# Kernel tuning notes

Hardware: AMD Instinct MI355X
Metric: run time of the kernel (lower is better)

Reference implementation:

```python
import jax, jax.numpy as jnp
import numpy as np
import math

def setup_inputs() -> dict:
    key = jax.random.key(0)
    qkv = jax.random.normal(key, (64, 192, 2048), dtype=jnp.float32)
    return {"qkv": qkv}

def reference(qkv):
    # qkv: [N, 3C, T]
    ch = qkv.shape[1] // 3
    q, k, v = jnp.split(qkv, 3, axis=1)  # each [N, C, T]
    scale = 1.0 / math.sqrt(math.sqrt(ch))
    # scores: [N, T, S]
    weight = jnp.einsum('bct,bcs->bts', q * scale, k * scale)
    weight = jax.nn.softmax(weight.astype(jnp.float32), axis=-1).astype(qkv.dtype)
    return jnp.einsum('bts,bcs->bct', weight, v)  # [N, C, T]
```

## Files before the change

### kernel.cpp

```cpp
#include <hip/hip_runtime.h>
#include <hip/hip_bf16.h>

typedef __attribute__((ext_vector_type(16))) float    f32x16;
typedef __attribute__((ext_vector_type(8)))  short    s16x8;
typedef __attribute__((ext_vector_type(2)))  unsigned u32x2;

#define NB    64
#define CH    64
#define TS    2048
#define QBLK  256
#define KVB   64
#define NKV   (TS / KVB)
#define KT_OFF  (16u * 1024 * 1024)
#define V_OFF   (32u * 1024 * 1024)
#define BSTRIDE (TS * CH * 2)
#define QSCALE  0.18033688011112042f

__device__ __forceinline__ unsigned f2bf(float f) {
    unsigned u = __float_as_uint(f);
    return (u + 0x7fffu + ((u >> 16) & 1u)) >> 16;
}
__device__ __forceinline__ unsigned cvtpk(float lo, float hi) {
    unsigned r;
    asm("v_cvt_pk_bf16_f32 %0, %1, %2" : "=v"(r) : "v"(lo), "v"(hi));
    return r;
}
__device__ __forceinline__ u32x2 plswap(unsigned x, unsigned y) {
#if __has_builtin(__builtin_amdgcn_permlane32_swap)
    return __builtin_amdgcn_permlane32_swap(x, y, false, false);
#else
    asm("v_permlane32_swap_b32 %0, %1" : "+v"(x), "+v"(y));
    u32x2 r; r.x = x; r.y = y; return r;
#endif
}
__device__ __forceinline__ float crosshalf_sum(float x) {
    const u32x2 r = plswap(__float_as_uint(x), __float_as_uint(x));
    return __uint_as_float(r.x) + __uint_as_float(r.y);
}
__device__ __forceinline__ void gload16(const void* g, void* l) {
    __builtin_amdgcn_global_load_lds(
        (const __attribute__((address_space(1))) void*)g,
        (__attribute__((address_space(3))) void*)l, 16, 0, 0);
}

__global__ __launch_bounds__(256)
void prep_all(const float* __restrict__ qkv, char* __restrict__ ws)
{
    __shared__ float tile[64][65];
    const int bid = (int)blockIdx.x;
    if (bid < NB * 32) {
        const int b  = bid >> 5;
        const int tt = bid & 31;
        const float* src = qkv + ((size_t)b * 192 + 64) * TS + tt * 64;

        const int c  = threadIdx.x >> 2;
        const int tq = (threadIdx.x & 3) * 16;
        const float4* s4 = (const float4*)(src + (size_t)c * TS + tq);
        #pragma unroll
        for (int j = 0; j < 4; ++j) {
            const float4 f = s4[j];
            tile[c][tq + 4*j + 0] = f.x;
            tile[c][tq + 4*j + 1] = f.y;
            tile[c][tq + 4*j + 2] = f.z;
            tile[c][tq + 4*j + 3] = f.w;
        }
        __syncthreads();

        const int t  = threadIdx.x >> 2;
        const int cq = (threadIdx.x & 3) * 16;
        unsigned pk[8];
        #pragma unroll
        for (int j = 0; j < 8; ++j) {
            const float f0 = tile[cq + 2*j][t];
            const float f1 = tile[cq + 2*j + 1][t];
            pk[j] = f2bf(f0) | (f2bf(f1) << 16);
        }
        char* dst = ws + KT_OFF +
                    (size_t)b * BSTRIDE + ((size_t)tt * 64 + t) * 128 + cq * 2;
        ((uint4*)dst)[0] = make_uint4(pk[0], pk[1], pk[2], pk[3]);
        ((uint4*)dst)[1] = make_uint4(pk[4], pk[5], pk[6], pk[7]);
    } else {
        const size_t e   = ((size_t)(bid - NB * 32) * 256 + threadIdx.x) * 16;
        const int b      = (int)(e >> 17);
        const size_t rem = e & 131071;
        const float4* src = (const float4*)(qkv + (size_t)b * 393216 + 262144 + rem);
        unsigned pk[8];
        #pragma unroll
        for (int j = 0; j < 4; ++j) {
            const float4 f = src[j];
            pk[2*j]     = f2bf(f.x) | (f2bf(f.y) << 16);
            pk[2*j + 1] = f2bf(f.z) | (f2bf(f.w) << 16);
        }
        char* dst = ws + V_OFF + e * 2;
        ((uint4*)dst)[0] = make_uint4(pk[0], pk[1], pk[2], pk[3]);
        ((uint4*)dst)[1] = make_uint4(pk[4], pk[5], pk[6], pk[7]);
    }
}

template<bool DIRA>
__device__ __forceinline__ void attn_main(
    const float* __restrict__ qsrcB, const char* __restrict__ ktb,
    const char* __restrict__ vtb, float* __restrict__ ob,
    char* k_sm0, char* k_sm1, char* v_sm0, char* v_sm1,
    int t0, int lane, int wv, int tid)
{
    const int col = lane & 31;
    const int hi  = lane >> 5;

    const int rowb = tid >> 3;
    const unsigned offX = (unsigned)(((tid & 7) ^ (rowb & 7)) << 4);
    const char* ksrc = ktb + rowb * 128  + offX;
    const char* vsrc = vtb + rowb * 4096 + offX;
    char* kd0 = k_sm0 + tid * 16;
    char* vd0 = v_sm0 + tid * 16;
    char* kd1 = k_sm1 + tid * 16;
    char* vd1 = v_sm1 + tid * 16;

    gload16(ksrc, kd0);
    gload16(vsrc, vd0);

    s16x8 qfrag[4];
    {
        const int t = t0 + wv * 32 + col;
        const float* qs = qsrcB + t;
        #pragma unroll
        for (int ks = 0; ks < 4; ++ks) {
            union { unsigned u[4]; s16x8 v; } qq;
            #pragma unroll
            for (int m = 0; m < 4; ++m) {
                const int c = ks * 16 + hi * 8 + 2 * m;
                const float a = qs[(size_t)c * TS]       * QSCALE;
                const float b = qs[(size_t)(c + 1) * TS] * QSCALE;
                qq.u[m] = cvtpk(a, b);
            }
            qfrag[ks] = qq.v;
        }
    }

    f32x16 zf;
    f32x16 oacc0, oacc1;
    #pragma unroll
    for (int i = 0; i < 16; ++i) { zf[i] = 0.f; oacc0[i] = 0.f; oacc1[i] = 0.f; }
    float l_run = 0.f;

    __syncthreads();

    int cur = 0;
    for (int kt = 0; kt < NKV; ++kt) {
        if (kt + 1 < NKV) {
            gload16(ksrc + (size_t)(kt + 1) * 8192, cur ? kd0 : kd1);
            gload16(vsrc + (size_t)(kt + 1) * 128,  cur ? vd0 : vd1);
        }
        const char* kb = cur ? k_sm1 : k_sm0;
        const char* vb = cur ? v_sm1 : v_sm0;

        f32x16 sa0, sa1;
        __builtin_amdgcn_s_setprio(1);
        #pragma unroll
        for (int ks = 0; ks < 4; ++ks) {
            const int sw = 32 * ks + 16 * hi;
            const s16x8 kf0 = *(const s16x8*)(kb + col * 128        + (sw ^ ((col & 7) << 4)));
            const s16x8 kf1 = *(const s16x8*)(kb + (32 + col) * 128 + (sw ^ ((col & 7) << 4)));
            if (ks == 0) {
                sa0 = __builtin_amdgcn_mfma_f32_32x32x16_bf16(kf0, qfrag[0], zf, 0, 0, 0);
                sa1 = __builtin_amdgcn_mfma_f32_32x32x16_bf16(kf1, qfrag[0], zf, 0, 0, 0);
            } else {
                sa0 = __builtin_amdgcn_mfma_f32_32x32x16_bf16(kf0, qfrag[ks], sa0, 0, 0, 0);
                sa1 = __builtin_amdgcn_mfma_f32_32x32x16_bf16(kf1, qfrag[ks], sa1, 0, 0, 0);
            }
        }
        __builtin_amdgcn_s_setprio(0);

        unsigned pq0[8], pq1[8];
        float s0 = 0.f, s1 = 0.f, s2 = 0.f, s3 = 0.f;
        #pragma unroll
        for (int q = 0; q < 8; ++q) {
            const float e0 = __builtin_amdgcn_exp2f(sa0[2*q]);
            const float e1 = __builtin_amdgcn_exp2f(sa0[2*q + 1]);
            const float f0 = __builtin_amdgcn_exp2f(sa1[2*q]);
            const float f1 = __builtin_amdgcn_exp2f(sa1[2*q + 1]);
            s0 += e0; s1 += e1; s2 += f0; s3 += f1;
            pq0[q] = cvtpk(e0, e1);
            pq1[q] = cvtpk(f0, f1);
        }
        l_run += (s0 + s1) + (s2 + s3);

        __builtin_amdgcn_s_setprio(1);
        #pragma unroll
        for (int ks = 0; ks < 4; ++ks) {
            const int base = (ks & 1) * 4;
            unsigned a0, a1, a2, a3;
            if (ks < 2) { a0 = pq0[base]; a1 = pq0[base+1]; a2 = pq0[base+2]; a3 = pq0[base+3]; }
            else        { a0 = pq1[base]; a1 = pq1[base+1]; a2 = pq1[base+2]; a3 = pq1[base+3]; }
            unsigned u0, u1, u2, u3;
            if (DIRA) {
                const u32x2 r02 = plswap(a0, a2), r13 = plswap(a1, a3);
                u0 = r02.x; u2 = r02.y; u1 = r13.x; u3 = r13.y;
            } else {
                const u32x2 r02 = plswap(a2, a0), r13 = plswap(a3, a1);
                u0 = r02.y; u2 = r02.x; u1 = r13.y; u3 = r13.x;
            }
            union { unsigned u[4]; s16x8 v; } pb;
            pb.u[0] = u0; pb.u[1] = u1; pb.u[2] = u2; pb.u[3] = u3;
            const int sw = 32 * ks + 16 * hi;
            const s16x8 vf0 = *(const s16x8*)(vb + col * 128        + (sw ^ ((col & 7) << 4)));
            const s16x8 vf1 = *(const s16x8*)(vb + (32 + col) * 128 + (sw ^ ((col & 7) << 4)));
            oacc0 = __builtin_amdgcn_mfma_f32_32x32x16_bf16(vf0, pb.v, oacc0, 0, 0, 0);
            oacc1 = __builtin_amdgcn_mfma_f32_32x32x16_bf16(vf1, pb.v, oacc1, 0, 0, 0);
        }
        __builtin_amdgcn_s_setprio(0);
        __syncthreads();
        cur ^= 1;
    }

    const float inv = 1.0f / crosshalf_sum(l_run);
    const int t = t0 + wv * 32 + col;
    #pragma unroll
    for (int r = 0; r < 16; ++r) {
        const int c = (r & 3) + 8 * (r >> 2) + 4 * hi;
        ob[(size_t)c * TS + t]        = oacc0[r] * inv;
        ob[(size_t)(c + 32) * TS + t] = oacc1[r] * inv;
    }
}

__global__ __launch_bounds__(512, 4)
void qkv_attn_kernel(const float* __restrict__ qkv, const char* __restrict__ ws,
                     float* __restrict__ out)
{
    __shared__ __align__(16) char k_sm[2][KVB * 128];
    __shared__ __align__(16) char v_sm[2][CH * 128];

    const int tid  = threadIdx.x;
    const int lane = tid & 63;
    const int wv   = tid >> 6;

    const u32x2 pr = plswap((unsigned)lane, 100u + (unsigned)lane);
    const bool dirA = (__builtin_amdgcn_readfirstlane((int)pr.x) == 0);

    const int Dd      = (int)blockIdx.x;
    const int logical = (Dd & 7) * 64 + (Dd >> 3);
    const int b  = logical >> 3;
    const int qt = logical & 7;
    const int t0 = qt * QBLK;

    const float* qsrcB = qkv + (size_t)b * 192 * TS;
    const char* ktb = ws + KT_OFF + (size_t)b * BSTRIDE;
    const char* vtb = ws + V_OFF  + (size_t)b * BSTRIDE;
    float* ob       = out + (size_t)b * CH * TS;

    if (dirA)
        attn_main<true >(qsrcB, ktb, vtb, ob, k_sm[0], k_sm[1], v_sm[0], v_sm[1], t0, lane, wv, tid);
    else
        attn_main<false>(qsrcB, ktb, vtb, ob, k_sm[0], k_sm[1], v_sm[0], v_sm[1], t0, lane, wv, tid);
}

extern "C" void kernel_launch(void* const* d_in, const int* in_sizes, int n_in,
                              void* d_out, int out_size, void* d_ws, size_t ws_size,
                              hipStream_t stream) {
    const float* qkv = (const float*)d_in[0];
    float* outp      = (float*)d_out;
    char* ws         = (char*)d_ws;
    prep_all<<<dim3(NB * 32 + 2048), dim3(256), 0, stream>>>(qkv, ws);
    qkv_attn_kernel<<<dim3(NB * (TS / QBLK)), dim3(512), 0, stream>>>(qkv, ws, outp);
}
```

Baseline: 96.94 us.

## Double KV tile to 128 and stage V through registers into LDS

Raises the KV block from 64 to 128 tokens, so each loop iteration runs two 64-token sub-steps and the number of __syncthreads barriers and loop overheads is halved. V tiles are now loaded from global memory into registers early in the iteration and written to the other LDS buffer after compute, instead of using direct global-to-LDS loads. K still uses gload16 with two loads per thread. Shared memory per block grows from 32KB to 64KB. That may cut resident blocks per CU below the launch-bounds target of 4, and the register-held V data adds register pressure.

```diff
diff --git a/kernel.cpp b/kernel.cpp
--- a/kernel.cpp
+++ b/kernel.cpp
@@ -9,7 +9,7 @@
 #define CH    64
 #define TS    2048
 #define QBLK  256
-#define KVB   64
+#define KVB   128
 #define NKV   (TS / KVB)
 #define KT_OFF  (16u * 1024 * 1024)
 #define V_OFF   (32u * 1024 * 1024)
@@ -101,23 +101,29 @@
 __device__ __forceinline__ void attn_main(
     const float* __restrict__ qsrcB, const char* __restrict__ ktb,
     const char* __restrict__ vtb, float* __restrict__ ob,
-    char* k_sm0, char* k_sm1, char* v_sm0, char* v_sm1,
-    int t0, int lane, int wv, int tid)
+    char* sm, int t0, int lane, int wv, int tid)
 {
     const int col = lane & 31;
     const int hi  = lane >> 5;
 
-    const int rowb = tid >> 3;
-    const unsigned offX = (unsigned)(((tid & 7) ^ (rowb & 7)) << 4);
-    const char* ksrc = ktb + rowb * 128  + offX;
-    const char* vsrc = vtb + rowb * 4096 + offX;
-    char* kd0 = k_sm0 + tid * 16;
-    char* vd0 = v_sm0 + tid * 16;
-    char* kd1 = k_sm1 + tid * 16;
-    char* vd1 = v_sm1 + tid * 16;
-
-    gload16(ksrc, kd0);
-    gload16(vsrc, vd0);
+    char* kbuf0 = sm;
+    char* kbuf1 = sm + 16384;
+    char* vbuf0 = sm + 32768;
+    char* vbuf1 = sm + 49152;
+
+    const int rowK = tid >> 3;
+    const unsigned offK = (unsigned)(((tid & 7) << 4) ^ ((rowK & 7) << 4));
+    const char* ksrc = ktb + rowK * 128 + offK;
+    char* kd0 = kbuf0 + tid * 16;
+    char* kd1 = kbuf1 + tid * 16;
+
+    const int rowV = tid >> 4;
+    const unsigned offV = (unsigned)(((tid & 15) << 4) ^ ((rowV & 7) << 4));
+    const char* vsrc = vtb + rowV * 4096 + offV;
+
+    uint4 vreg1 = *(const uint4*)(vsrc);
+    uint4 vreg2 = *(const uint4*)(vsrc + 131072);
+    gload16(ksrc, kd0);            gload16(ksrc + 8192, kd0 + 8192);
 
     s16x8 qfrag[4];
     {
@@ -143,72 +149,89 @@
     for (int i = 0; i < 16; ++i) { zf[i] = 0.f; oacc0[i] = 0.f; oacc1[i] = 0.f; }
     float l_run = 0.f;
 
+    *(uint4*)(vbuf0 + tid * 16)        = vreg1;
+    *(uint4*)(vbuf0 + tid * 16 + 8192) = vreg2;
     __syncthreads();
 
     int cur = 0;
     for (int kt = 0; kt < NKV; ++kt) {
         if (kt + 1 < NKV) {
-            gload16(ksrc + (size_t)(kt + 1) * 8192, cur ? kd0 : kd1);
-            gload16(vsrc + (size_t)(kt + 1) * 128,  cur ? vd0 : vd1);
-        }
-        const char* kb = cur ? k_sm1 : k_sm0;
-        const char* vb = cur ? v_sm1 : v_sm0;
-
-        f32x16 sa0, sa1;
-        __builtin_amdgcn_s_setprio(1);
-        #pragma unroll
-        for (int ks = 0; ks < 4; ++ks) {
-            const int sw = 32 * ks + 16 * hi;
-            const s16x8 kf0 = *(const s16x8*)(kb + col * 128        + (sw ^ ((col & 7) << 4)));
-            const s16x8 kf1 = *(const s16x8*)(kb + (32 + col) * 128 + (sw ^ ((col & 7) << 4)));
-            if (ks == 0) {
-                sa0 = __builtin_amdgcn_mfma_f32_32x32x16_bf16(kf0, qfrag[0], zf, 0, 0, 0);
-                sa1 = __builtin_amdgcn_mfma_f32_32x32x16_bf16(kf1, qfrag[0], zf, 0, 0, 0);
-            } else {
-                sa0 = __builtin_amdgcn_mfma_f32_32x32x16_bf16(kf0, qfrag[ks], sa0, 0, 0, 0);
-                sa1 = __builtin_amdgcn_mfma_f32_32x32x16_bf16(kf1, qfrag[ks], sa1, 0, 0, 0);
-            }
-        }
-        __builtin_amdgcn_s_setprio(0);
-
-        unsigned pq0[8], pq1[8];
-        float s0 = 0.f, s1 = 0.f, s2 = 0.f, s3 = 0.f;
-        #pragma unroll
-        for (int q = 0; q < 8; ++q) {
-            const float e0 = __builtin_amdgcn_exp2f(sa0[2*q]);
-            const float e1 = __builtin_amdgcn_exp2f(sa0[2*q + 1]);
-            const float f0 = __builtin_amdgcn_exp2f(sa1[2*q]);
-            const float f1 = __builtin_amdgcn_exp2f(sa1[2*q + 1]);
-            s0 += e0; s1 += e1; s2 += f0; s3 += f1;
-            pq0[q] = cvtpk(e0, e1);
-            pq1[q] = cvtpk(f0, f1);
-        }
-        l_run += (s0 + s1) + (s2 + s3);
-
-        __builtin_amdgcn_s_setprio(1);
-        #pragma unroll
-        for (int ks = 0; ks < 4; ++ks) {
-            const int base = (ks & 1) * 4;
-            unsigned a0, a1, a2, a3;
-            if (ks < 2) { a0 = pq0[base]; a1 = pq0[base+1]; a2 = pq0[base+2]; a3 = pq0[base+3]; }
-            else        { a0 = pq1[base]; a1 = pq1[base+1]; a2 = pq1[base+2]; a3 = pq1[base+3]; }
-            unsigned u0, u1, u2, u3;
-            if (DIRA) {
-                const u32x2 r02 = plswap(a0, a2), r13 = plswap(a1, a3);
-                u0 = r02.x; u2 = r02.y; u1 = r13.x; u3 = r13.y;
-            } else {
-                const u32x2 r02 = plswap(a2, a0), r13 = plswap(a3, a1);
-                u0 = r02.y; u2 = r02.x; u1 = r13.y; u3 = r13.x;
-            }
-            union { unsigned u[4]; s16x8 v; } pb;
-            pb.u[0] = u0; pb.u[1] = u1; pb.u[2] = u2; pb.u[3] = u3;
-            const int sw = 32 * ks + 16 * hi;
-            const s16x8 vf0 = *(const s16x8*)(vb + col * 128        + (sw ^ ((col & 7) << 4)));
-            const s16x8 vf1 = *(const s16x8*)(vb + (32 + col) * 128 + (sw ^ ((col & 7) << 4)));
-            oacc0 = __builtin_amdgcn_mfma_f32_32x32x16_bf16(vf0, pb.v, oacc0, 0, 0, 0);
-            oacc1 = __builtin_amdgcn_mfma_f32_32x32x16_bf16(vf1, pb.v, oacc1, 0, 0, 0);
-        }
-        __builtin_amdgcn_s_setprio(0);
+            const char* vp = vsrc + (size_t)(kt + 1) * 256;
+            vreg1 = *(const uint4*)(vp);
+            vreg2 = *(const uint4*)(vp + 131072);
+            const char* kp = ksrc + (size_t)(kt + 1) * 16384;
+            char* kd = cur ? kd0 : kd1;
+            gload16(kp, kd);           gload16(kp + 8192, kd + 8192);
+        }
+        const char* kb = cur ? kbuf1 : kbuf0;
+        const char* vb = cur ? vbuf1 : vbuf0;
+
+        #pragma unroll
+        for (int h = 0; h < 2; ++h) {
+            const char* kbh = kb + h * 8192;
+
+            f32x16 sa0, sa1;
+            __builtin_amdgcn_s_setprio(1);
+            #pragma unroll
+            for (int ks = 0; ks < 4; ++ks) {
+                const int sw = 32 * ks + 16 * hi;
+                const s16x8 kf0 = *(const s16x8*)(kbh + col * 128        + (sw ^ ((col & 7) << 4)));
+                const s16x8 kf1 = *(const s16x8*)(kbh + (32 + col) * 128 + (sw ^ ((col & 7) << 4)));
+                if (ks == 0) {
+                    sa0 = __builtin_amdgcn_mfma_f32_32x32x16_bf16(kf0, qfrag[0], zf, 0, 0, 0);
+                    sa1 = __builtin_amdgcn_mfma_f32_32x32x16_bf16(kf1, qfrag[0], zf, 0, 0, 0);
+                } else {
+                    sa0 = __builtin_amdgcn_mfma_f32_32x32x16_bf16(kf0, qfrag[ks], sa0, 0, 0, 0);
+                    sa1 = __builtin_amdgcn_mfma_f32_32x32x16_bf16(kf1, qfrag[ks], sa1, 0, 0, 0);
+                }
+            }
+            __builtin_amdgcn_s_setprio(0);
+
+            unsigned pq0[8], pq1[8];
+            float s0 = 0.f, s1 = 0.f, s2 = 0.f, s3 = 0.f;
+            #pragma unroll
+            for (int q = 0; q < 8; ++q) {
+                const float e0 = __builtin_amdgcn_exp2f(sa0[2*q]);
+                const float e1 = __builtin_amdgcn_exp2f(sa0[2*q + 1]);
+                const float f0 = __builtin_amdgcn_exp2f(sa1[2*q]);
+                const float f1 = __builtin_amdgcn_exp2f(sa1[2*q + 1]);
+                s0 += e0; s1 += e1; s2 += f0; s3 += f1;
+                pq0[q] = cvtpk(e0, e1);
+                pq1[q] = cvtpk(f0, f1);
+            }
+            l_run += (s0 + s1) + (s2 + s3);
+
+            __builtin_amdgcn_s_setprio(1);
+            #pragma unroll
+            for (int ks = 0; ks < 4; ++ks) {
+                const int base = (ks & 1) * 4;
+                unsigned a0, a1, a2, a3;
+                if (ks < 2) { a0 = pq0[base]; a1 = pq0[base+1]; a2 = pq0[base+2]; a3 = pq0[base+3]; }
+                else        { a0 = pq1[base]; a1 = pq1[base+1]; a2 = pq1[base+2]; a3 = pq1[base+3]; }
+                unsigned u0, u1, u2, u3;
+                if (DIRA) {
+                    const u32x2 r02 = plswap(a0, a2), r13 = plswap(a1, a3);
+                    u0 = r02.x; u2 = r02.y; u1 = r13.x; u3 = r13.y;
+                } else {
+                    const u32x2 r02 = plswap(a2, a0), r13 = plswap(a3, a1);
+                    u0 = r02.y; u2 = r02.x; u1 = r13.y; u3 = r13.x;
+                }
+                union { unsigned u[4]; s16x8 v; } pb;
+                pb.u[0] = u0; pb.u[1] = u1; pb.u[2] = u2; pb.u[3] = u3;
+                const int loff = h * 128 + 32 * ks + 16 * hi;
+                const s16x8 vf0 = *(const s16x8*)(vb + col * 256        + (loff ^ ((col & 7) << 4)));
+                const s16x8 vf1 = *(const s16x8*)(vb + (32 + col) * 256 + (loff ^ ((col & 7) << 4)));
+                oacc0 = __builtin_amdgcn_mfma_f32_32x32x16_bf16(vf0, pb.v, oacc0, 0, 0, 0);
+                oacc1 = __builtin_amdgcn_mfma_f32_32x32x16_bf16(vf1, pb.v, oacc1, 0, 0, 0);
+            }
+            __builtin_amdgcn_s_setprio(0);
+        }
+
+        if (kt + 1 < NKV) {
+            char* vd = cur ? vbuf0 : vbuf1;
+            *(uint4*)(vd + tid * 16)        = vreg1;
+            *(uint4*)(vd + tid * 16 + 8192) = vreg2;
+        }
         __syncthreads();
         cur ^= 1;
     }
@@ -227,8 +250,7 @@
 void qkv_attn_kernel(const float* __restrict__ qkv, const char* __restrict__ ws,
                      float* __restrict__ out)
 {
-    __shared__ __align__(16) char k_sm[2][KVB * 128];
-    __shared__ __align__(16) char v_sm[2][CH * 128];
+    __shared__ __align__(16) char sm[65536];
 
     const int tid  = threadIdx.x;
     const int lane = tid & 63;
@@ -249,9 +271,9 @@
     float* ob       = out + (size_t)b * CH * TS;
 
     if (dirA)
-        attn_main<true >(qsrcB, ktb, vtb, ob, k_sm[0], k_sm[1], v_sm[0], v_sm[1], t0, lane, wv, tid);
+        attn_main<true >(qsrcB, ktb, vtb, ob, sm, t0, lane, wv, tid);
     else
-        attn_main<false>(qsrcB, ktb, vtb, ob, k_sm[0], k_sm[1], v_sm[0], v_sm[1], t0, lane, wv, tid);
+        attn_main<false>(qsrcB, ktb, vtb, ob, sm, t0, lane, wv, tid);
 }
 
 extern "C" void kernel_launch(void* const* d_in, const int* in_sizes, int n_in,
```

Result: slower. 103.0 us (+6.2%).
